# Kernel tuning notes

Measured on AMD Instinct MI355X. Metric: run time of the kernel, lower is better.

## Reference

```python
import jax, jax.numpy as jnp
import numpy as np

LAYER_SPECS = [(2, 4, 1), (2, 4, 1), (1, 4, 1), (1, 4, 1)]
SKIPS = [(k - s) * d for (s, k, d) in LAYER_SPECS]  # (ksz-stride)*dilation
C = 80  # encoder channels


def _conv1d(x, w, b, stride, dilation):
    # x: (N, Cin, L), w: (Cout, Cin, K)
    out = jax.lax.conv_general_dilated(
        x, w, window_strides=(stride,), padding='VALID',
        rhs_dilation=(dilation,), dimension_numbers=('NCH', 'OIH', 'NCH'))
    return out + b[None, :, None]


def _encoder(x, w_wide, b_wide, w_1x1, b_1x1, w_f0, b_f0, w_f1, b_f1):
    # x: (N, T, 80) -> (N, T', 80)
    x = jnp.transpose(x, (0, 2, 1))  # (N, 80, T)
    for i, ((stride, ksz, dil), skip) in enumerate(zip(LAYER_SPECS, SKIPS)):
        x1 = _conv1d(x, w_wide[i], b_wide[i], stride, dil)  # (N, 2C, L')
        a, g = jnp.split(x1, 2, axis=1)
        x2 = jnp.tanh(a) * jax.nn.sigmoid(g)                # gated activation
        x3 = _conv1d(x2, w_1x1[i], b_1x1[i], 1, 1)          # (N, C, L')
        if i == 0:
            x = x3
        else:
            T3 = x3.shape[2]
            # residual: strided slice of previous x, take last of each stride group
            res = x[:, :, skip:skip + T3 * stride].reshape(x.shape[0], C, T3, stride)[:, :, :, -1]
            x = x3 + res
    x = _conv1d(jax.nn.relu(_conv1d(x, w_f0, b_f0, 1, 1)), w_f1, b_f1, 1, 1)
    return jnp.transpose(x, (0, 2, 1))  # (N, T', 80)


def setup_inputs() -> dict:
    key = jax.random.key(0)
    ks = jax.random.split(key, 10)
    N, Ts, Tq = 16, 8192, 2048
    return {
        'search': jax.random.normal(ks[0], (N, Ts, 80), dtype=jnp.float32),
        'query': jax.random.normal(ks[1], (N, Tq, 80), dtype=jnp.float32),
        'w_wide': jax.random.normal(ks[2], (4, 160, 80, 4), dtype=jnp.float32) * 0.02,
        'b_wide': jnp.zeros((4, 160), dtype=jnp.float32),
        'w_1x1': jax.random.normal(ks[3], (4, 80, 80, 1), dtype=jnp.float32) * 0.05,
        'b_1x1': jnp.zeros((4, 80), dtype=jnp.float32),
        'w_f0': jax.random.normal(ks[4], (80, 80, 1), dtype=jnp.float32) * 0.05,
        'b_f0': jnp.zeros((80,), dtype=jnp.float32),
        'w_f1': jax.random.normal(ks[5], (80, 80, 1), dtype=jnp.float32) * 0.05,
        'b_f1': jax.random.normal(ks[6], (80,), dtype=jnp.float32) * 0.05,
        'embedding': jax.random.normal(ks[7], (1, 512, 80), dtype=jnp.float32) * 0.001,
        'w_lin': jax.random.normal(ks[8], (2, 80), dtype=jnp.float32) * 0.05,
        'b_lin': jnp.zeros((2,), dtype=jnp.float32),
    }


def reference(search, query, w_wide, b_wide, w_1x1, b_1x1,
              w_f0, b_f0, w_f1, b_f1, embedding, w_lin, b_lin):
    enc_s = _encoder(search, w_wide, b_wide, w_1x1, b_1x1, w_f0, b_f0, w_f1, b_f1)
    enc_q = _encoder(query, w_wide, b_wide, w_1x1, b_1x1, w_f0, b_f0, w_f1, b_f1)

    # ---- VectorQuant (no normalize): nearest-codeword lookup + straight-through ----
    x = enc_s[:, :, None, :]                  # (N, T, 1, V)
    N, T, nc, V = x.shape
    n_classes = embedding.shape[1]
    x1 = x.reshape(N * T, nc, V)              # (NT, 1, V)
    # squared-distance via expansion: argmin identical to argmin of L2 norm
    x2 = jnp.sum(x1 * x1, axis=-1, keepdims=True)          # (NT, 1, 1)
    e2 = jnp.sum(embedding * embedding, axis=-1)[None]     # (1, 1, K)
    xe = jnp.einsum('ncv,ckv->nck', x1, embedding)         # (NT, 1, K)
    idx = jnp.argmin(x2 - 2.0 * xe + e2, axis=2)           # (NT, 1)
    offset = jnp.arange(nc) * n_classes
    flat = embedding.reshape(-1, V)
    output = flat[(idx + offset[None, :]).reshape(-1)].reshape(x.shape)
    out0 = jax.lax.stop_gradient(output - x) + x           # straight-through
    discrete = out0[:, :, 0, :]               # (N, Ts', V)

    # ---- align query to search length, classify, max-pool over time ----
    sf = discrete.shape[1] // enc_q.shape[1]
    q = jnp.tile(enc_q, (1, sf, 1))
    pad = discrete.shape[1] - q.shape[1]
    q = jnp.pad(q, ((0, 0), (0, pad), (0, 0)))
    pred = jnp.tanh((q + discrete) @ w_lin.T + b_lin)      # (N, Ts', 2)
    return jnp.max(pred, axis=1)                           # (N, 2)
```

## Files before the change

### kernel.cpp

```cpp
#include <hip/hip_runtime.h>
#include <math.h>


#define NBATCH 16

typedef __attribute__((ext_vector_type(8))) short s16x8;
typedef __attribute__((ext_vector_type(4))) float f32x4;

__device__ __forceinline__ float fast_sigmoid(float x){ return 1.0f/(1.0f+__expf(-x)); }
__device__ __forceinline__ float fast_tanh(float x){ return 2.0f/(1.0f+__expf(-2.0f*x))-1.0f; }
__device__ __forceinline__ unsigned short f2bf(float f){
    unsigned int u = __float_as_uint(f);
    return (unsigned short)((u + 0x7FFFu + ((u >> 16) & 1u)) >> 16);
}
__device__ __forceinline__ unsigned int pk2bf(float lo, float hi){
    unsigned int r;
    asm("v_cvt_pk_bf16_f32 %0, %1, %2" : "=v"(r) : "v"(lo), "v"(hi));
    return r;
}

__global__ __launch_bounds__(256) void pack_all(
    const float* __restrict__ w_wide, const float* __restrict__ w_1x1,
    const float* __restrict__ wf0,    const float* __restrict__ wf1,
    const float* __restrict__ emb,
    unsigned short* __restrict__ WW, unsigned short* __restrict__ W1,
    unsigned short* __restrict__ F0, unsigned short* __restrict__ F1,
    unsigned short* __restrict__ EM, float* __restrict__ e2o)
{
    int i = blockIdx.x * 256 + threadIdx.x;
    if (i < 204800) {
        int l = i / 51200, r = i % 51200, oc = r / 320, k = r % 320;
        int j = k / 80, ic = k % 80;
        WW[i] = f2bf(w_wide[l * 51200 + oc * 320 + ic * 4 + j]);
    } else if (i < 235520) {
        int idx = i - 204800, l = idx / 7680, r = idx % 7680, oc = r / 96, k = r % 96;
        W1[idx] = (k < 80) ? f2bf(w_1x1[l * 6400 + oc * 80 + k]) : (unsigned short)0;
    } else if (i < 243200) {
        int idx = i - 235520, oc = idx / 96, k = idx % 96;
        F0[idx] = (k < 80) ? f2bf(wf0[oc * 80 + k]) : (unsigned short)0;
    } else if (i < 250880) {
        int idx = i - 243200, oc = idx / 96, k = idx % 96;
        F1[idx] = (k < 80) ? f2bf(wf1[oc * 80 + k]) : (unsigned short)0;
    } else if (i < 291840) {
        EM[i - 250880] = f2bf(emb[i - 250880]);
    } else if (i < 292352) {
        int e = i - 291840;
        float s = 0.f;
        for (int k = 0; k < 80; ++k) { float v = emb[e * 80 + k]; s = fmaf(v, v, s); }
        e2o[e] = s;
    }
}

template<int S, bool HAS_RES, bool FINAL>
__global__ __launch_bounds__(320, 2) void enc_layer(
    const float* __restrict__ xS, const float* __restrict__ xQ,
    const unsigned short* __restrict__ ww,  const float* __restrict__ wb,
    const unsigned short* __restrict__ w1p, const float* __restrict__ b1,
    const unsigned short* __restrict__ f0p, const float* __restrict__ bf0,
    const unsigned short* __restrict__ f1p, const float* __restrict__ bf1,
    float* __restrict__ outS, float* __restrict__ outQ,
    int TinS, int ToutS, int TinQ, int ToutQ, int nbS)
{
    constexpr int TILE = 64;
    constexpr int MT   = 4;
    constexpr int P    = 63 * S + 4;
    constexpr int HALF = (S == 2) ? 65 : 67;
    constexpr int NPARY = (S == 2) ? 2 : 1;
    constexpr int XSTR = 104;
    constexpr int NEL  = P * 20;
    constexpr int NST  = (NEL + 319) / 320;

    __shared__ __attribute__((aligned(16))) unsigned short xs[NPARY * HALF * XSTR];
    __shared__ __attribute__((aligned(16))) unsigned short gsA[TILE * 104];
    __shared__ __attribute__((aligned(16))) unsigned short gsB[FINAL ? TILE * 104 : 8];

    const int tid  = threadIdx.x;
    const int wave = tid >> 6;
    const int lane = tid & 63;
    const int m    = lane & 15;
    const int quad = lane >> 4;
    const int n_   = blockIdx.y;

    const float* x; float* out; int T_in, T_out, bx;
    if ((int)blockIdx.x < nbS) { x = xS; out = outS; T_in = TinS; T_out = ToutS; bx = blockIdx.x; }
    else                       { x = xQ; out = outQ; T_in = TinQ; T_out = ToutQ; bx = blockIdx.x - nbS; }
    const int t0 = bx * TILE;
    const long base_in = (long)n_ * T_in * 80;

    float4 vst[NST]; int odx[NST]; bool okw[NST];
#pragma unroll
    for (int it = 0; it < NST; ++it) {
        int u = tid + it * 320;
        okw[it] = (u < NEL);
        if (u >= NEL) u = NEL - 1;
        int pos = u / 20, c4 = u % 20;
        int tp = t0 * S + pos; if (tp > T_in - 1) tp = T_in - 1;
        vst[it] = *(const float4*)(x + base_in + (long)tp * 80 + c4 * 4);
        int row = (S == 2) ? (pos >> 1) : pos;
        int par = (S == 2) ? (pos & 1) : 0;
        odx[it] = (par * HALF + row) * XSTR + c4 * 4;
    }

    const int quad8 = quad * 8;
    const unsigned short* wa_base = ww + (long)(wave * 16 + m) * 320 + quad8;
    const unsigned short* wg_base = ww + (long)((wave + 5) * 16 + m) * 320 + quad8;
    s16x8 wA[10], wG[10];
#pragma unroll
    for (int kk = 0; kk < 10; ++kk) {
        wA[kk] = *(const s16x8*)(wa_base + kk * 32);
        wG[kk] = *(const s16x8*)(wg_base + kk * 32);
    }
    const unsigned short* wb1 = w1p + (long)(wave * 16 + m) * 96 + quad8;
    s16x8 w1b0 = *(const s16x8*)(wb1);
    s16x8 w1b1 = *(const s16x8*)(wb1 + 32);
    s16x8 w1b2 = *(const s16x8*)(wb1 + 64);
    const float ba_b = wb[wave * 16 + m];
    const float bg_b = wb[80 + wave * 16 + m];
    const int c = wave * 16 + m;
    const float b1c = b1[c];

#pragma unroll
    for (int it = 0; it < NST; ++it) {
        if (okw[it]) {
            float4 v = vst[it];
            *(uint2*)&xs[odx[it]] = make_uint2(pk2bf(v.x, v.y), pk2bf(v.z, v.w));
        }
    }

    f32x4 acc_a[MT], acc_g[MT];
#pragma unroll
    for (int mt = 0; mt < MT; ++mt) {
        acc_a[mt] = (f32x4){0.f, 0.f, 0.f, 0.f};
        acc_g[mt] = (f32x4){0.f, 0.f, 0.f, 0.f};
    }

    __syncthreads();

#pragma unroll
    for (int kk = 0; kk < 10; ++kk) {
        const int kq = kk * 32 + quad8;
        const int j  = (kq >= 240) ? 3 : ((kq >= 160) ? 2 : ((kq >= 80) ? 1 : 0));
        const int ic0 = kq - j * 80;
        int xb;
        if (S == 2) xb = ((j & 1) * HALF + (j >> 1)) * XSTR + ic0;
        else        xb = j * XSTR + ic0;
        s16x8 a[MT];
#pragma unroll
        for (int mt = 0; mt < MT; ++mt)
            a[mt] = *(const s16x8*)&xs[xb + (mt * 16 + m) * XSTR];
#pragma unroll
        for (int mt = 0; mt < MT; ++mt) {
            acc_a[mt] = __builtin_amdgcn_mfma_f32_16x16x32_bf16(a[mt], wA[kk], acc_a[mt], 0, 0, 0);
            acc_g[mt] = __builtin_amdgcn_mfma_f32_16x16x32_bf16(a[mt], wG[kk], acc_g[mt], 0, 0, 0);
        }
    }

#pragma unroll
    for (int mt = 0; mt < MT; ++mt)
#pragma unroll
        for (int r = 0; r < 4; ++r) {
            float av = acc_a[mt][r] + ba_b;
            float gv = acc_g[mt][r] + bg_b;
            gsA[(mt * 16 + quad * 4 + r) * 104 + c] =
                f2bf(fast_tanh(av) * fast_sigmoid(gv));
        }
    const uint4 z4 = make_uint4(0u, 0u, 0u, 0u);
    {
        constexpr int NPAD = FINAL ? 256 : 128;
        for (int u = tid; u < NPAD; u += 320) {
            unsigned short* g = (u < 128) ? gsA : gsB;
            int v = u & 127;
            *(uint4*)&g[(v >> 1) * 104 + 80 + (v & 1) * 8] = z4;
        }
    }
    __syncthreads();

    auto mm96 = [&](s16x8 b0, s16x8 b1f, s16x8 b2, const unsigned short* g, f32x4 (&o)[MT]) {
#pragma unroll
        for (int mt = 0; mt < MT; ++mt) o[mt] = (f32x4){0.f, 0.f, 0.f, 0.f};
#pragma unroll
        for (int kb = 0; kb < 3; ++kb) {
            s16x8 b = (kb == 0) ? b0 : ((kb == 1) ? b1f : b2);
#pragma unroll
            for (int mt = 0; mt < MT; ++mt) {
                s16x8 ag = *(const s16x8*)&g[(mt * 16 + m) * 104 + kb * 32 + quad8];
                o[mt] = __builtin_amdgcn_mfma_f32_16x16x32_bf16(ag, b, o[mt], 0, 0, 0);
            }
        }
    };

    f32x4 a1[MT];
    mm96(w1b0, w1b1, w1b2, gsA, a1);

    const long base_out = (long)n_ * T_out * 80;
    if (!FINAL) {
#pragma unroll
        for (int mt = 0; mt < MT; ++mt)
#pragma unroll
            for (int r = 0; r < 4; ++r) {
                int tg = t0 + mt * 16 + quad * 4 + r;
                if (tg < T_out) {
                    float v = a1[mt][r] + b1c;
                    if (HAS_RES)
                        v += x[base_in + (long)(3 + (long)tg * S) * 80 + c];
                    out[base_out + (long)tg * 80 + c] = v;
                }
            }
    } else {
        float x3[MT][4];
#pragma unroll
        for (int mt = 0; mt < MT; ++mt)
#pragma unroll
            for (int r = 0; r < 4; ++r) {
                int tg = t0 + mt * 16 + quad * 4 + r;
                int tc = (tg < T_out) ? tg : (T_out - 1);
                float v = a1[mt][r] + b1c;
                if (HAS_RES)
                    v += x[base_in + (long)(3 + (long)tc * S) * 80 + c];
                x3[mt][r] = v;
            }
        const unsigned short* wf0b = f0p + (long)c * 96 + quad8;
        s16x8 f0b0 = *(const s16x8*)(wf0b);
        s16x8 f0b1 = *(const s16x8*)(wf0b + 32);
        s16x8 f0b2 = *(const s16x8*)(wf0b + 64);
        const float bf0c = bf0[c];
#pragma unroll
        for (int mt = 0; mt < MT; ++mt)
#pragma unroll
            for (int r = 0; r < 4; ++r)
                gsB[(mt * 16 + quad * 4 + r) * 104 + c] = f2bf(x3[mt][r]);
        __syncthreads();
        f32x4 a2[MT];
        mm96(f0b0, f0b1, f0b2, gsB, a2);
        const unsigned short* wf1b = f1p + (long)c * 96 + quad8;
        s16x8 f1b0 = *(const s16x8*)(wf1b);
        s16x8 f1b1 = *(const s16x8*)(wf1b + 32);
        s16x8 f1b2 = *(const s16x8*)(wf1b + 64);
        const float bf1c = bf1[c];
#pragma unroll
        for (int mt = 0; mt < MT; ++mt)
#pragma unroll
            for (int r = 0; r < 4; ++r)
                gsA[(mt * 16 + quad * 4 + r) * 104 + c] =
                    f2bf(fmaxf(a2[mt][r] + bf0c, 0.f));
        __syncthreads();
        f32x4 a3[MT];
        mm96(f1b0, f1b1, f1b2, gsA, a3);
#pragma unroll
        for (int mt = 0; mt < MT; ++mt)
#pragma unroll
            for (int r = 0; r < 4; ++r) {
                int tg = t0 + mt * 16 + quad * 4 + r;
                if (tg < T_out)
                    out[base_out + (long)tg * 80 + c] = a3[mt][r] + bf1c;
            }
    }
}

__global__ __launch_bounds__(256, 2) void vq_mfma(
    const float* __restrict__ enc_s, const float* __restrict__ enc_q,
    const unsigned short* __restrict__ embp, const float* __restrict__ emb,
    const float* __restrict__ e2v,
    const float* __restrict__ w_lin, const float* __restrict__ b_lin,
    float* __restrict__ pred)
{
    __shared__ unsigned short xs[64 * 104];
    __shared__ unsigned short es[128 * 104];
    const uint4 z4 = make_uint4(0u, 0u, 0u, 0u);

    const int tid  = threadIdx.x;
    const int wave = tid >> 6;
    const int lane = tid & 63;
    const int m    = lane & 15;
    const int quad = lane >> 4;
    const int n    = blockIdx.y;
    const int t0   = blockIdx.x * 64;

    for (int u = tid; u < 64 * 20; u += 256) {
        int row = u / 20, c4 = u % 20;
        int t = t0 + row; if (t > 2039) t = 2039;
        float4 v = *(const float4*)(enc_s + ((long)n * 2040 + t) * 80 + c4 * 4);
        unsigned int s0 = (unsigned int)f2bf(v.x) | ((unsigned int)f2bf(v.y) << 16);
        unsigned int s1 = (unsigned int)f2bf(v.z) | ((unsigned int)f2bf(v.w) << 16);
        *(uint2*)&xs[row * 104 + c4 * 4] = make_uint2(s0, s1);
    }
    for (int u = tid; u < 128; u += 256)
        *(uint4*)&xs[(u >> 1) * 104 + 80 + (u & 1) * 8] = z4;
    __syncthreads();

    s16x8 af[3];
#pragma unroll
    for (int kb = 0; kb < 3; ++kb)
        af[kb] = *(const s16x8*)&xs[(wave * 16 + m) * 104 + kb * 32 + quad * 8];

    float best[4]; int bi[4];
#pragma unroll
    for (int r = 0; r < 4; ++r) { best[r] = 1e30f; bi[r] = 0; }

    for (int ch = 0; ch < 4; ++ch) {
        const int c0 = ch * 128;
        __syncthreads();
        for (int u = tid; u < 128 * 12; u += 256) {
            int el = u / 12, seg = u % 12;
            uint4 v = z4;
            if (seg < 10) v = *(const uint4*)(embp + (long)(c0 + el) * 80 + seg * 8);
            *(uint4*)&es[el * 104 + seg * 8] = v;
        }
        __syncthreads();

        f32x4 acc[8];
#pragma unroll
        for (int nt = 0; nt < 8; ++nt) acc[nt] = (f32x4){0.f, 0.f, 0.f, 0.f};
#pragma unroll
        for (int kb = 0; kb < 3; ++kb) {
            const int k0 = kb * 32 + quad * 8;
#pragma unroll
            for (int nt = 0; nt < 8; ++nt) {
                s16x8 b = *(const s16x8*)&es[(nt * 16 + m) * 104 + k0];
                acc[nt] = __builtin_amdgcn_mfma_f32_16x16x32_bf16(af[kb], b, acc[nt], 0, 0, 0);
            }
        }
#pragma unroll
        for (int nt = 0; nt < 8; ++nt) {
            const int e = c0 + nt * 16 + m;
            const float e2x = e2v[e];
#pragma unroll
            for (int r = 0; r < 4; ++r) {
                float s = fmaf(-2.0f, acc[nt][r], e2x);
                if (s < best[r]) { best[r] = s; bi[r] = e; }
            }
        }
    }

    __syncthreads();
    float* rb = (float*)es;
    int*   ri = (int*)es + 1088;
#pragma unroll
    for (int r = 0; r < 4; ++r) {
        int tl = wave * 16 + quad * 4 + r;
        rb[tl * 17 + m] = best[r];
        ri[tl * 17 + m] = bi[r];
    }
    __syncthreads();

    if (tid < 64) {
        const int t = t0 + tid;
        float b = rb[tid * 17]; int ix = ri[tid * 17];
#pragma unroll
        for (int j = 1; j < 16; ++j) {
            float v = rb[tid * 17 + j]; int iv = ri[tid * 17 + j];
            if (v < b || (v == b && iv < ix)) { b = v; ix = iv; }
        }
        if (t < 2040) {
            const float4* ev = (const float4*)(emb + (long)ix * 80);
            const bool hasq = (t < 2016);
            const float4* qv = hasq
                ? (const float4*)(enc_q + ((long)n * 504 + (t % 504)) * 80) : nullptr;
            float p0 = b_lin[0], p1 = b_lin[1];
#pragma unroll
            for (int i = 0; i < 20; ++i) {
                float4 e4 = ev[i];
                float4 q4 = hasq ? qv[i] : make_float4(0.f, 0.f, 0.f, 0.f);
                float4 w0 = *(const float4*)(w_lin + 4 * i);
                float4 w1 = *(const float4*)(w_lin + 80 + 4 * i);
                float sx = e4.x + q4.x, sy = e4.y + q4.y;
                float sz = e4.z + q4.z, sw = e4.w + q4.w;
                p0 = fmaf(sx, w0.x, p0); p1 = fmaf(sx, w1.x, p1);
                p0 = fmaf(sy, w0.y, p0); p1 = fmaf(sy, w1.y, p1);
                p0 = fmaf(sz, w0.z, p0); p1 = fmaf(sz, w1.z, p1);
                p0 = fmaf(sw, w0.w, p0); p1 = fmaf(sw, w1.w, p1);
            }
            long o = ((long)n * 2040 + t) * 2;
            pred[o]     = fast_tanh(p0);
            pred[o + 1] = fast_tanh(p1);
        }
    }
}

__global__ __launch_bounds__(256) void max_red(const float* __restrict__ pred,
                                               float* __restrict__ out)
{
    __shared__ float s0[256], s1[256];
    const int n = blockIdx.x, tid = threadIdx.x;
    float m0 = -1e30f, m1 = -1e30f;
    for (int t = tid; t < 2040; t += 256) {
        long o = ((long)n * 2040 + t) * 2;
        m0 = fmaxf(m0, pred[o]);
        m1 = fmaxf(m1, pred[o + 1]);
    }
    s0[tid] = m0; s1[tid] = m1;
    __syncthreads();
    for (int st = 128; st > 0; st >>= 1) {
        if (tid < st) {
            s0[tid] = fmaxf(s0[tid], s0[tid + st]);
            s1[tid] = fmaxf(s1[tid], s1[tid + st]);
        }
        __syncthreads();
    }
    if (tid == 0) { out[n * 2] = s0[0]; out[n * 2 + 1] = s1[0]; }
}

extern "C" void kernel_launch(void* const* d_in, const int* in_sizes, int n_in,
                              void* d_out, int out_size, void* d_ws, size_t ws_size,
                              hipStream_t stream)
{
    const float* search = (const float*)d_in[0];
    const float* query  = (const float*)d_in[1];
    const float* w_wide = (const float*)d_in[2];
    const float* b_wide = (const float*)d_in[3];
    const float* w_1x1  = (const float*)d_in[4];
    const float* b_1x1  = (const float*)d_in[5];
    const float* w_f0   = (const float*)d_in[6];
    const float* b_f0   = (const float*)d_in[7];
    const float* w_f1   = (const float*)d_in[8];
    const float* b_f1   = (const float*)d_in[9];
    const float* emb    = (const float*)d_in[10];
    const float* w_lin  = (const float*)d_in[11];
    const float* b_lin  = (const float*)d_in[12];
    float* out = (float*)d_out;
    float* ws  = (float*)d_ws;

    float* A  = ws;
    float* B  = A  + 5241600;
    float* C  = B  + 2618880;
    float* QA = C  + 2618880;
    float* QB = QA + 1309440;
    float* QC = QB + 652800;
    unsigned short* WWp = (unsigned short*)(QC + 652800);
    unsigned short* W1p = WWp + 204800;
    unsigned short* F0p = W1p + 30720;
    unsigned short* F1p = F0p + 7680;
    unsigned short* EMp = F1p + 7680;
    float* e2b = (float*)(EMp + 40960);

    const dim3 blk(320);
    auto nb = [](int T) { return (T + 63) / 64; };

    pack_all<<<dim3(1142), dim3(256), 0, stream>>>(w_wide, w_1x1, w_f0, w_f1, emb,
                                                   WWp, W1p, F0p, F1p, EMp, e2b);

    enc_layer<2, false, false><<<dim3(nb(4095) + nb(1023), NBATCH), blk, 0, stream>>>(
        search, query, WWp, b_wide, W1p, b_1x1, nullptr, nullptr, nullptr, nullptr,
        A, QA, 8192, 4095, 2048, 1023, nb(4095));
    enc_layer<2, true, false><<<dim3(nb(2046) + nb(510), NBATCH), blk, 0, stream>>>(
        A, QA, WWp + 51200, b_wide + 160, W1p + 7680, b_1x1 + 80,
        nullptr, nullptr, nullptr, nullptr,
        B, QB, 4095, 2046, 1023, 510, nb(2046));
    enc_layer<1, true, false><<<dim3(nb(2043) + nb(507), NBATCH), blk, 0, stream>>>(
        B, QB, WWp + 102400, b_wide + 320, W1p + 15360, b_1x1 + 160,
        nullptr, nullptr, nullptr, nullptr,
        C, QC, 2046, 2043, 510, 507, nb(2043));
    enc_layer<1, true, true><<<dim3(nb(2040) + nb(504), NBATCH), blk, 0, stream>>>(
        C, QC, WWp + 153600, b_wide + 480, W1p + 23040, b_1x1 + 240,
        F0p, b_f0, F1p, b_f1,
        B, QB, 2043, 2040, 507, 504, nb(2040));

    vq_mfma<<<dim3(32, NBATCH), dim3(256), 0, stream>>>(B, QB, EMp, emb, e2b,
                                                        w_lin, b_lin, C);
    max_red<<<dim3(NBATCH), dim3(256), 0, stream>>>(C, out);
}
```

Measured before the change: 267.4 us.

## Make encoder layers persistent with double-buffered input prefetch and streamed weights

Encoder layer kernels now launch a fixed grid of 512 blocks that loop over (batch, time-tile) jobs. Each block prefetches the next tile's input into registers during the tail of the current MFMA loop and converts it into a second shared buffer, overlapping global loads with compute. Wide-conv weights are streamed through a 3-slot register ring instead of being held as 20 registers, the input tile stride shrinks to 88, and the gate buffer aliases the input buffer. Together these target 3 blocks per CU and less load latency, at the cost of extra synchronisation and possible load imbalance at the end of the job list.

```diff
diff --git a/kernel.cpp b/kernel.cpp
--- a/kernel.cpp
+++ b/kernel.cpp
@@ -52,208 +52,271 @@
 }
 
 template<int S, bool HAS_RES, bool FINAL>
-__global__ __launch_bounds__(320, 2) void enc_layer(
+__global__ __launch_bounds__(320, 3) void enc_layer(
     const float* __restrict__ xS, const float* __restrict__ xQ,
     const unsigned short* __restrict__ ww,  const float* __restrict__ wb,
     const unsigned short* __restrict__ w1p, const float* __restrict__ b1,
     const unsigned short* __restrict__ f0p, const float* __restrict__ bf0,
     const unsigned short* __restrict__ f1p, const float* __restrict__ bf1,
     float* __restrict__ outS, float* __restrict__ outQ,
-    int TinS, int ToutS, int TinQ, int ToutQ, int nbS)
+    int TinS, int ToutS, int TinQ, int ToutQ, int nbS, int nbT, int njobs)
 {
-    constexpr int TILE = 64;
     constexpr int MT   = 4;
     constexpr int P    = 63 * S + 4;
     constexpr int HALF = (S == 2) ? 65 : 67;
-    constexpr int NPARY = (S == 2) ? 2 : 1;
-    constexpr int XSTR = 104;
+    constexpr int NPARY= (S == 2) ? 2 : 1;
+    constexpr int XSH  = NPARY * HALF * 88;
+    constexpr int GSH  = 64 * 104;
+    constexpr int BUF  = (XSH > GSH) ? XSH : GSH;
     constexpr int NEL  = P * 20;
     constexpr int NST  = (NEL + 319) / 320;
 
-    __shared__ __attribute__((aligned(16))) unsigned short xs[NPARY * HALF * XSTR];
-    __shared__ __attribute__((aligned(16))) unsigned short gsA[TILE * 104];
-    __shared__ __attribute__((aligned(16))) unsigned short gsB[FINAL ? TILE * 104 : 8];
+    __shared__ __attribute__((aligned(16))) unsigned short Xs[2][BUF];
+    __shared__ __attribute__((aligned(16))) unsigned short gsB[FINAL ? GSH : 8];
 
     const int tid  = threadIdx.x;
     const int wave = tid >> 6;
     const int lane = tid & 63;
     const int m    = lane & 15;
     const int quad = lane >> 4;
-    const int n_   = blockIdx.y;
-
-    const float* x; float* out; int T_in, T_out, bx;
-    if ((int)blockIdx.x < nbS) { x = xS; out = outS; T_in = TinS; T_out = ToutS; bx = blockIdx.x; }
-    else                       { x = xQ; out = outQ; T_in = TinQ; T_out = ToutQ; bx = blockIdx.x - nbS; }
-    const int t0 = bx * TILE;
-    const long base_in = (long)n_ * T_in * 80;
-
-    float4 vst[NST]; int odx[NST]; bool okw[NST];
-#pragma unroll
-    for (int it = 0; it < NST; ++it) {
-        int u = tid + it * 320;
-        okw[it] = (u < NEL);
-        if (u >= NEL) u = NEL - 1;
-        int pos = u / 20, c4 = u % 20;
-        int tp = t0 * S + pos; if (tp > T_in - 1) tp = T_in - 1;
-        vst[it] = *(const float4*)(x + base_in + (long)tp * 80 + c4 * 4);
-        int row = (S == 2) ? (pos >> 1) : pos;
-        int par = (S == 2) ? (pos & 1) : 0;
-        odx[it] = (par * HALF + row) * XSTR + c4 * 4;
-    }
-
     const int quad8 = quad * 8;
+    const int c    = wave * 16 + m;
+
+    int job = blockIdx.x;
+    if (job >= njobs) return;
+
     const unsigned short* wa_base = ww + (long)(wave * 16 + m) * 320 + quad8;
     const unsigned short* wg_base = ww + (long)((wave + 5) * 16 + m) * 320 + quad8;
-    s16x8 wA[10], wG[10];
-#pragma unroll
-    for (int kk = 0; kk < 10; ++kk) {
-        wA[kk] = *(const s16x8*)(wa_base + kk * 32);
-        wG[kk] = *(const s16x8*)(wg_base + kk * 32);
-    }
-    const unsigned short* wb1 = w1p + (long)(wave * 16 + m) * 96 + quad8;
+    auto ldB = [&](const unsigned short* b, int kk) { return *(const s16x8*)(b + kk * 32); };
+    const unsigned short* wb1 = w1p + (long)c * 96 + quad8;
     s16x8 w1b0 = *(const s16x8*)(wb1);
     s16x8 w1b1 = *(const s16x8*)(wb1 + 32);
     s16x8 w1b2 = *(const s16x8*)(wb1 + 64);
-    const float ba_b = wb[wave * 16 + m];
-    const float bg_b = wb[80 + wave * 16 + m];
-    const int c = wave * 16 + m;
-    const float b1c = b1[c];
-
-#pragma unroll
-    for (int it = 0; it < NST; ++it) {
-        if (okw[it]) {
-            float4 v = vst[it];
-            *(uint2*)&xs[odx[it]] = make_uint2(pk2bf(v.x, v.y), pk2bf(v.z, v.w));
-        }
-    }
-
-    f32x4 acc_a[MT], acc_g[MT];
-#pragma unroll
-    for (int mt = 0; mt < MT; ++mt) {
-        acc_a[mt] = (f32x4){0.f, 0.f, 0.f, 0.f};
-        acc_g[mt] = (f32x4){0.f, 0.f, 0.f, 0.f};
-    }
-
+    const float ba_b = wb[c];
+    const float bg_b = wb[80 + c];
+    const float b1c  = b1[c];
+
+    auto decode = [&](int j, const float*& x, float*& out, int& T_in, int& T_out, int& t0) {
+        int n = j / nbT, r = j - n * nbT;
+        if (r < nbS) {
+            x = xS + (long)n * TinS * 80; out = outS + (long)n * ToutS * 80;
+            T_in = TinS; T_out = ToutS; t0 = r * 64;
+        } else {
+            x = xQ + (long)n * TinQ * 80; out = outQ + (long)n * ToutQ * 80;
+            T_in = TinQ; T_out = ToutQ; t0 = (r - nbS) * 64;
+        }
+    };
+
+    auto issue_stage = [&](const float* x, int T_in, int t0, float4 (&v)[NST]) {
+#pragma unroll
+        for (int it = 0; it < NST; ++it) {
+            int u = tid + it * 320;
+            if (u >= NEL) u = NEL - 1;
+            int pos = u / 20, c4 = u % 20;
+            int tp = t0 * S + pos; if (tp > T_in - 1) tp = T_in - 1;
+            v[it] = *(const float4*)(x + (long)tp * 80 + c4 * 4);
+        }
+    };
+    auto do_convert = [&](unsigned short* xbuf, float4 (&v)[NST]) {
+#pragma unroll
+        for (int it = 0; it < NST; ++it) {
+            int u = tid + it * 320;
+            if (u < NEL) {
+                int pos = u / 20, c4 = u % 20;
+                int row = (S == 2) ? (pos >> 1) : pos;
+                int par = (S == 2) ? (pos & 1) : 0;
+                int o = (par * HALF + row) * 88 + c4 * 4;
+                *(uint2*)&xbuf[o] = make_uint2(pk2bf(v[it].x, v[it].y),
+                                               pk2bf(v[it].z, v[it].w));
+            }
+        }
+    };
+
+    const float* cx; float* cout_; int cTin, cTout, ct0;
+    decode(job, cx, cout_, cTin, cTout, ct0);
+    float4 vst[NST];
+    issue_stage(cx, cTin, ct0, vst);
+    do_convert(Xs[0], vst);
     __syncthreads();
 
-#pragma unroll
-    for (int kk = 0; kk < 10; ++kk) {
-        const int kq = kk * 32 + quad8;
-        const int j  = (kq >= 240) ? 3 : ((kq >= 160) ? 2 : ((kq >= 80) ? 1 : 0));
-        const int ic0 = kq - j * 80;
-        int xb;
-        if (S == 2) xb = ((j & 1) * HALF + (j >> 1)) * XSTR + ic0;
-        else        xb = j * XSTR + ic0;
-        s16x8 a[MT];
+    int p = 0;
+    s16x8 baP[3], bgP[3];
+    baP[0] = ldB(wa_base, 0); bgP[0] = ldB(wg_base, 0);
+    baP[1] = ldB(wa_base, 1); bgP[1] = ldB(wg_base, 1);
+
+    const uint4 z4 = make_uint4(0u, 0u, 0u, 0u);
+
+    while (true) {
+        const int nxt = job + (int)gridDim.x;
+        const bool have_next = (nxt < njobs);
+        const float* nx = nullptr; float* nout = nullptr; int nTin = 0, nTout = 0, nt0 = 0;
+
+        f32x4 acc_a[MT], acc_g[MT];
+#pragma unroll
+        for (int mt = 0; mt < MT; ++mt) {
+            acc_a[mt] = (f32x4){0.f, 0.f, 0.f, 0.f};
+            acc_g[mt] = (f32x4){0.f, 0.f, 0.f, 0.f};
+        }
+
+        const unsigned short* xs = Xs[p];
+#pragma unroll
+        for (int kk = 0; kk < 8; ++kk) {
+            baP[(kk + 2) % 3] = ldB(wa_base, kk + 2);
+            bgP[(kk + 2) % 3] = ldB(wg_base, kk + 2);
+            const int kq = kk * 32 + quad8;
+            const int j  = (kq >= 240) ? 3 : ((kq >= 160) ? 2 : ((kq >= 80) ? 1 : 0));
+            const int ic0 = kq - j * 80;
+            int xb;
+            if (S == 2) xb = ((j & 1) * HALF + (j >> 1)) * 88 + ic0;
+            else        xb = j * 88 + ic0;
+            s16x8 a[MT];
+#pragma unroll
+            for (int mt = 0; mt < MT; ++mt)
+                a[mt] = *(const s16x8*)&xs[xb + (mt * 16 + m) * 88];
+            s16x8 ba = baP[kk % 3], bg = bgP[kk % 3];
+#pragma unroll
+            for (int mt = 0; mt < MT; ++mt) {
+                acc_a[mt] = __builtin_amdgcn_mfma_f32_16x16x32_bf16(a[mt], ba, acc_a[mt], 0, 0, 0);
+                acc_g[mt] = __builtin_amdgcn_mfma_f32_16x16x32_bf16(a[mt], bg, acc_g[mt], 0, 0, 0);
+            }
+        }
+
+        if (have_next) {
+            decode(nxt, nx, nout, nTin, nTout, nt0);
+            issue_stage(nx, nTin, nt0, vst);
+        }
+
+#pragma unroll
+        for (int kk = 8; kk < 10; ++kk) {
+            const int kq = kk * 32 + quad8;
+            const int j  = (kq >= 240) ? 3 : ((kq >= 160) ? 2 : ((kq >= 80) ? 1 : 0));
+            const int ic0 = kq - j * 80;
+            int xb;
+            if (S == 2) xb = ((j & 1) * HALF + (j >> 1)) * 88 + ic0;
+            else        xb = j * 88 + ic0;
+            s16x8 a[MT];
+#pragma unroll
+            for (int mt = 0; mt < MT; ++mt)
+                a[mt] = *(const s16x8*)&xs[xb + (mt * 16 + m) * 88];
+            s16x8 ba = baP[kk % 3], bg = bgP[kk % 3];
+#pragma unroll
+            for (int mt = 0; mt < MT; ++mt) {
+                acc_a[mt] = __builtin_amdgcn_mfma_f32_16x16x32_bf16(a[mt], ba, acc_a[mt], 0, 0, 0);
+                acc_g[mt] = __builtin_amdgcn_mfma_f32_16x16x32_bf16(a[mt], bg, acc_g[mt], 0, 0, 0);
+            }
+        }
+
+        __syncthreads();
+
+        unsigned short* G = Xs[p];
 #pragma unroll
         for (int mt = 0; mt < MT; ++mt)
-            a[mt] = *(const s16x8*)&xs[xb + (mt * 16 + m) * XSTR];
-#pragma unroll
-        for (int mt = 0; mt < MT; ++mt) {
-            acc_a[mt] = __builtin_amdgcn_mfma_f32_16x16x32_bf16(a[mt], wA[kk], acc_a[mt], 0, 0, 0);
-            acc_g[mt] = __builtin_amdgcn_mfma_f32_16x16x32_bf16(a[mt], wG[kk], acc_g[mt], 0, 0, 0);
-        }
-    }
-
-#pragma unroll
-    for (int mt = 0; mt < MT; ++mt)
-#pragma unroll
-        for (int r = 0; r < 4; ++r) {
-            float av = acc_a[mt][r] + ba_b;
-            float gv = acc_g[mt][r] + bg_b;
-            gsA[(mt * 16 + quad * 4 + r) * 104 + c] =
-                f2bf(fast_tanh(av) * fast_sigmoid(gv));
-        }
-    const uint4 z4 = make_uint4(0u, 0u, 0u, 0u);
-    {
-        constexpr int NPAD = FINAL ? 256 : 128;
-        for (int u = tid; u < NPAD; u += 320) {
-            unsigned short* g = (u < 128) ? gsA : gsB;
-            int v = u & 127;
-            *(uint4*)&g[(v >> 1) * 104 + 80 + (v & 1) * 8] = z4;
-        }
-    }
-    __syncthreads();
-
-    auto mm96 = [&](s16x8 b0, s16x8 b1f, s16x8 b2, const unsigned short* g, f32x4 (&o)[MT]) {
-#pragma unroll
-        for (int mt = 0; mt < MT; ++mt) o[mt] = (f32x4){0.f, 0.f, 0.f, 0.f};
-#pragma unroll
-        for (int kb = 0; kb < 3; ++kb) {
-            s16x8 b = (kb == 0) ? b0 : ((kb == 1) ? b1f : b2);
-#pragma unroll
-            for (int mt = 0; mt < MT; ++mt) {
-                s16x8 ag = *(const s16x8*)&g[(mt * 16 + m) * 104 + kb * 32 + quad8];
-                o[mt] = __builtin_amdgcn_mfma_f32_16x16x32_bf16(ag, b, o[mt], 0, 0, 0);
-            }
-        }
-    };
-
-    f32x4 a1[MT];
-    mm96(w1b0, w1b1, w1b2, gsA, a1);
-
-    const long base_out = (long)n_ * T_out * 80;
-    if (!FINAL) {
-#pragma unroll
-        for (int mt = 0; mt < MT; ++mt)
 #pragma unroll
             for (int r = 0; r < 4; ++r) {
-                int tg = t0 + mt * 16 + quad * 4 + r;
-                if (tg < T_out) {
+                float av = acc_a[mt][r] + ba_b;
+                float gv = acc_g[mt][r] + bg_b;
+                G[(mt * 16 + quad * 4 + r) * 104 + c] =
+                    f2bf(fast_tanh(av) * fast_sigmoid(gv));
+            }
+        {
+            constexpr int NPAD = FINAL ? 256 : 128;
+            for (int u = tid; u < NPAD; u += 320) {
+                unsigned short* g = (u < 128) ? G : gsB;
+                int v = u & 127;
+                *(uint4*)&g[(v >> 1) * 104 + 80 + (v & 1) * 8] = z4;
+            }
+        }
+
+        if (have_next) do_convert(Xs[p ^ 1], vst);
+
+        baP[0] = ldB(wa_base, 0); bgP[0] = ldB(wg_base, 0);
+        baP[1] = ldB(wa_base, 1); bgP[1] = ldB(wg_base, 1);
+
+        __syncthreads();
+
+        auto mm96 = [&](s16x8 b0, s16x8 b1f, s16x8 b2, const unsigned short* g, f32x4 (&o)[MT]) {
+#pragma unroll
+            for (int mt = 0; mt < MT; ++mt) o[mt] = (f32x4){0.f, 0.f, 0.f, 0.f};
+#pragma unroll
+            for (int kb = 0; kb < 3; ++kb) {
+                s16x8 b = (kb == 0) ? b0 : ((kb == 1) ? b1f : b2);
+#pragma unroll
+                for (int mt = 0; mt < MT; ++mt) {
+                    s16x8 ag = *(const s16x8*)&g[(mt * 16 + m) * 104 + kb * 32 + quad8];
+                    o[mt] = __builtin_amdgcn_mfma_f32_16x16x32_bf16(ag, b, o[mt], 0, 0, 0);
+                }
+            }
+        };
+
+        f32x4 a1[MT];
+        mm96(w1b0, w1b1, w1b2, G, a1);
+
+        if (!FINAL) {
+#pragma unroll
+            for (int mt = 0; mt < MT; ++mt)
+#pragma unroll
+                for (int r = 0; r < 4; ++r) {
+                    int tg = ct0 + mt * 16 + quad * 4 + r;
+                    if (tg < cTout) {
+                        float v = a1[mt][r] + b1c;
+                        if (HAS_RES)
+                            v += cx[(long)(3 + (long)tg * S) * 80 + c];
+                        cout_[(long)tg * 80 + c] = v;
+                    }
+                }
+        } else {
+            float x3[MT][4];
+#pragma unroll
+            for (int mt = 0; mt < MT; ++mt)
+#pragma unroll
+                for (int r = 0; r < 4; ++r) {
+                    int tg = ct0 + mt * 16 + quad * 4 + r;
+                    int tc = (tg < cTout) ? tg : (cTout - 1);
                     float v = a1[mt][r] + b1c;
                     if (HAS_RES)
-                        v += x[base_in + (long)(3 + (long)tg * S) * 80 + c];
-                    out[base_out + (long)tg * 80 + c] = v;
+                        v += cx[(long)(3 + (long)tc * S) * 80 + c];
+                    x3[mt][r] = v;
                 }
-            }
-    } else {
-        float x3[MT][4];
-#pragma unroll
-        for (int mt = 0; mt < MT; ++mt)
-#pragma unroll
-            for (int r = 0; r < 4; ++r) {
-                int tg = t0 + mt * 16 + quad * 4 + r;
-                int tc = (tg < T_out) ? tg : (T_out - 1);
-                float v = a1[mt][r] + b1c;
-                if (HAS_RES)
-                    v += x[base_in + (long)(3 + (long)tc * S) * 80 + c];
-                x3[mt][r] = v;
-            }
-        const unsigned short* wf0b = f0p + (long)c * 96 + quad8;
-        s16x8 f0b0 = *(const s16x8*)(wf0b);
-        s16x8 f0b1 = *(const s16x8*)(wf0b + 32);
-        s16x8 f0b2 = *(const s16x8*)(wf0b + 64);
-        const float bf0c = bf0[c];
-#pragma unroll
-        for (int mt = 0; mt < MT; ++mt)
-#pragma unroll
-            for (int r = 0; r < 4; ++r)
-                gsB[(mt * 16 + quad * 4 + r) * 104 + c] = f2bf(x3[mt][r]);
-        __syncthreads();
-        f32x4 a2[MT];
-        mm96(f0b0, f0b1, f0b2, gsB, a2);
-        const unsigned short* wf1b = f1p + (long)c * 96 + quad8;
-        s16x8 f1b0 = *(const s16x8*)(wf1b);
-        s16x8 f1b1 = *(const s16x8*)(wf1b + 32);
-        s16x8 f1b2 = *(const s16x8*)(wf1b + 64);
-        const float bf1c = bf1[c];
-#pragma unroll
-        for (int mt = 0; mt < MT; ++mt)
-#pragma unroll
-            for (int r = 0; r < 4; ++r)
-                gsA[(mt * 16 + quad * 4 + r) * 104 + c] =
-                    f2bf(fmaxf(a2[mt][r] + bf0c, 0.f));
-        __syncthreads();
-        f32x4 a3[MT];
-        mm96(f1b0, f1b1, f1b2, gsA, a3);
-#pragma unroll
-        for (int mt = 0; mt < MT; ++mt)
-#pragma unroll
-            for (int r = 0; r < 4; ++r) {
-                int tg = t0 + mt * 16 + quad * 4 + r;
-                if (tg < T_out)
-                    out[base_out + (long)tg * 80 + c] = a3[mt][r] + bf1c;
-            }
+            const unsigned short* wf0b = f0p + (long)c * 96 + quad8;
+            s16x8 f0b0 = *(const s16x8*)(wf0b);
+            s16x8 f0b1 = *(const s16x8*)(wf0b + 32);
+            s16x8 f0b2 = *(const s16x8*)(wf0b + 64);
+            const float bf0c = bf0[c];
+#pragma unroll
+            for (int mt = 0; mt < MT; ++mt)
+#pragma unroll
+                for (int r = 0; r < 4; ++r)
+                    gsB[(mt * 16 + quad * 4 + r) * 104 + c] = f2bf(x3[mt][r]);
+            __syncthreads();
+            f32x4 a2[MT];
+            mm96(f0b0, f0b1, f0b2, gsB, a2);
+            const unsigned short* wf1b = f1p + (long)c * 96 + quad8;
+            s16x8 f1b0 = *(const s16x8*)(wf1b);
+            s16x8 f1b1 = *(const s16x8*)(wf1b + 32);
+            s16x8 f1b2 = *(const s16x8*)(wf1b + 64);
+            const float bf1c = bf1[c];
+#pragma unroll
+            for (int mt = 0; mt < MT; ++mt)
+#pragma unroll
+                for (int r = 0; r < 4; ++r)
+                    G[(mt * 16 + quad * 4 + r) * 104 + c] =
+                        f2bf(fmaxf(a2[mt][r] + bf0c, 0.f));
+            __syncthreads();
+            f32x4 a3[MT];
+            mm96(f1b0, f1b1, f1b2, G, a3);
+#pragma unroll
+            for (int mt = 0; mt < MT; ++mt)
+#pragma unroll
+                for (int r = 0; r < 4; ++r) {
+                    int tg = ct0 + mt * 16 + quad * 4 + r;
+                    if (tg < cTout)
+                        cout_[(long)tg * 80 + c] = a3[mt][r] + bf1c;
+                }
+        }
+
+        if (!have_next) break;
+        job = nxt; cx = nx; cout_ = nout; cTin = nTin; cTout = nTout; ct0 = nt0;
+        p ^= 1;
     }
 }
 
@@ -439,21 +502,33 @@
     pack_all<<<dim3(1142), dim3(256), 0, stream>>>(w_wide, w_1x1, w_f0, w_f1, emb,
                                                    WWp, W1p, F0p, F1p, EMp, e2b);
 
-    enc_layer<2, false, false><<<dim3(nb(4095) + nb(1023), NBATCH), blk, 0, stream>>>(
-        search, query, WWp, b_wide, W1p, b_1x1, nullptr, nullptr, nullptr, nullptr,
-        A, QA, 8192, 4095, 2048, 1023, nb(4095));
-    enc_layer<2, true, false><<<dim3(nb(2046) + nb(510), NBATCH), blk, 0, stream>>>(
-        A, QA, WWp + 51200, b_wide + 160, W1p + 7680, b_1x1 + 80,
-        nullptr, nullptr, nullptr, nullptr,
-        B, QB, 4095, 2046, 1023, 510, nb(2046));
-    enc_layer<1, true, false><<<dim3(nb(2043) + nb(507), NBATCH), blk, 0, stream>>>(
-        B, QB, WWp + 102400, b_wide + 320, W1p + 15360, b_1x1 + 160,
-        nullptr, nullptr, nullptr, nullptr,
-        C, QC, 2046, 2043, 510, 507, nb(2043));
-    enc_layer<1, true, true><<<dim3(nb(2040) + nb(504), NBATCH), blk, 0, stream>>>(
-        C, QC, WWp + 153600, b_wide + 480, W1p + 23040, b_1x1 + 240,
-        F0p, b_f0, F1p, b_f1,
-        B, QB, 2043, 2040, 507, 504, nb(2040));
+    {
+        int nbS_ = nb(4095), nbT_ = nb(4095) + nb(1023), nj = NBATCH * nbT_;
+        enc_layer<2, false, false><<<dim3(512), blk, 0, stream>>>(
+            search, query, WWp, b_wide, W1p, b_1x1, nullptr, nullptr, nullptr, nullptr,
+            A, QA, 8192, 4095, 2048, 1023, nbS_, nbT_, nj);
+    }
+    {
+        int nbS_ = nb(2046), nbT_ = nb(2046) + nb(510), nj = NBATCH * nbT_;
+        enc_layer<2, true, false><<<dim3(512), blk, 0, stream>>>(
+            A, QA, WWp + 51200, b_wide + 160, W1p + 7680, b_1x1 + 80,
+            nullptr, nullptr, nullptr, nullptr,
+            B, QB, 4095, 2046, 1023, 510, nbS_, nbT_, nj);
+    }
+    {
+        int nbS_ = nb(2043), nbT_ = nb(2043) + nb(507), nj = NBATCH * nbT_;
+        enc_layer<1, true, false><<<dim3(512), blk, 0, stream>>>(
+            B, QB, WWp + 102400, b_wide + 320, W1p + 15360, b_1x1 + 160,
+            nullptr, nullptr, nullptr, nullptr,
+            C, QC, 2046, 2043, 510, 507, nbS_, nbT_, nj);
+    }
+    {
+        int nbS_ = nb(2040), nbT_ = nb(2040) + nb(504), nj = NBATCH * nbT_;
+        enc_layer<1, true, true><<<dim3(512), blk, 0, stream>>>(
+            C, QC, WWp + 153600, b_wide + 480, W1p + 23040, b_1x1 + 240,
+            F0p, b_f0, F1p, b_f1,
+            B, QB, 2043, 2040, 507, 504, nbS_, nbT_, nj);
+    }
 
     vq_mfma<<<dim3(32, NBATCH), dim3(256), 0, stream>>>(B, QB, EMp, emb, e2b,
                                                         w_lin, b_lin, C);
```

Result: slower. 335.0 us (+25.3%).
